# Performance work log

Hardware: AMD Instinct MI355X
Metric: run time of the kernel (lower is better)

Reference implementation:

```python
import jax, jax.numpy as jnp
import numpy as np

B, T, D = 64, 32, 256
NFC = 2 * D          # num_inputs_fc = 512
DIMS = [4 * D, NFC, NFC // 2, NFC // 4, NFC // 8, 4]  # last layer padded to 4 outs
H = 4                # camera, rot, trans, plane heads stacked


def setup_inputs() -> dict:
    key = jax.random.key(0)
    ks = jax.random.split(key, 12)
    inp = {
        "emb": jax.random.normal(ks[0], (B, T, D), dtype=jnp.float32),
        # each of n0, n1 in [1,16] so n0+n1 <= T=32 and no divide-by-zero
        "num_planes": jax.random.randint(ks[1], (B, 2), 1, 17, dtype=jnp.int32),
    }
    for i in range(5):
        fan_in = DIMS[i]
        scale = 1.0 / np.sqrt(fan_in)
        inp[f"w{i}"] = jax.random.uniform(ks[2 + 2 * i], (H, DIMS[i], DIMS[i + 1]),
                                           minval=-scale, maxval=scale, dtype=jnp.float32)
        inp[f"b{i}"] = jax.random.uniform(ks[3 + 2 * i], (H, DIMS[i + 1]),
                                           minval=-scale, maxval=scale, dtype=jnp.float32)
    return inp


def _forward(emb, num_planes, w0, b0, w1, b1, w2, b2, w3, b3, w4, b4):
    Bs, Ts, Ds = emb.shape
    n0 = num_planes[:, 0]
    n1 = num_planes[:, 1]
    idx = jnp.arange(Ts)
    # img1 global feature: mean of tokens t < n0 (original zeroes t>=n0 then sums / n0)
    m1 = (idx[None, :] < n0[:, None])                                  # (B,T) bool
    g1 = (emb * m1[..., None].astype(emb.dtype)).sum(1) / n0[:, None].astype(emb.dtype)
    # img2 global feature: mean of tokens n0 <= t < n0+n1
    in2 = (idx[None, :] >= n0[:, None]) & (idx[None, :] < (n0 + n1)[:, None])  # (B,T)
    g2 = (emb * in2[..., None].astype(emb.dtype)).sum(1) / n1[:, None].astype(emb.dtype)
    # pairwise concat: [emb_i, emb_j, g1, g2] -> (B,T,T,4D)
    ei = jnp.broadcast_to(emb[:, :, None, :], (Bs, Ts, Ts, Ds))
    ej = jnp.broadcast_to(emb[:, None, :, :], (Bs, Ts, Ts, Ds))
    g1b = jnp.broadcast_to(g1[:, None, None, :], (Bs, Ts, Ts, Ds))
    g2b = jnp.broadcast_to(g2[:, None, None, :], (Bs, Ts, Ts, Ds))
    cat = jnp.concatenate([ei, ej, g1b, g2b], axis=-1)
    # 4 stacked MLP heads (camera, rot, trans, plane); final layer padded to 4 outputs
    h = jax.nn.relu(jnp.einsum('btsd,hdk->hbtsk', cat, w0) + b0[:, None, None, None, :])
    h = jax.nn.relu(jnp.einsum('hbtsd,hdk->hbtsk', h, w1) + b1[:, None, None, None, :])
    h = jax.nn.relu(jnp.einsum('hbtsd,hdk->hbtsk', h, w2) + b2[:, None, None, None, :])
    h = jax.nn.relu(jnp.einsum('hbtsd,hdk->hbtsk', h, w3) + b3[:, None, None, None, :])
    h = jnp.einsum('hbtsd,hdk->hbtsk', h, w4) + b4[:, None, None, None, :]  # (4,B,T,T,4)
    camera = h[0, ..., 0]            # (B,T,T)
    rot = h[1]                       # (B,T,T,4)
    trans = h[2, ..., :3]            # (B,T,T,3)
    plane_corr = jax.nn.sigmoid(h[3, ..., 0])  # (B,T,T)
    # valid pairs: row i < n0, col j in [n0, n0+n1)  (== ~padding_mask)
    valid = m1[:, :, None] & in2[:, None, :]                           # (B,T,T) bool
    v = valid.astype(emb.dtype)
    pf = (n0 * n1).astype(emb.dtype)
    camera_corr = jax.nn.sigmoid((camera * v).sum((1, 2)) / pf)        # (B,)
    rot_res = (rot * v[..., None]).sum((1, 2)) / pf[:, None]           # (B,4)
    trans_res = (trans * v[..., None]).sum((1, 2)) / pf[:, None]       # (B,3)
    return camera_corr, rot_res, trans_res, plane_corr, valid


def reference(emb, num_planes, w0, b0, w1, b1, w2, b2, w3, b3, w4, b4):
    return _forward(emb, num_planes, w0, b0, w1, b1, w2, b2, w3, b3, w4, b4)
```

## Files before the change

kernel.cpp:

```cpp
#include <hip/hip_runtime.h>

typedef float f32x4 __attribute__((ext_vector_type(4)));
typedef short short8 __attribute__((ext_vector_type(8)));
typedef unsigned short ushort_t;
typedef unsigned int uint_t;

constexpr int O_CAM   = 0;
constexpr int O_ROT   = 64;
constexpr int O_TRANS = 320;
constexpr int O_PLANE = 512;
constexpr int O_VALID = 66048;

constexpr size_t B_G1   = 0;
constexpr size_t B_G2   = 65536;
constexpr size_t B_ACC  = 131072;
constexpr size_t B_ABF  = 133120;
constexpr size_t B_CBF  = 8521728;
constexpr size_t B_BT1  = 16910336;
constexpr size_t B_BT2  = 17958912;
constexpr size_t B_BT3  = 18221056;
constexpr size_t B_BT0F = 18286592;

__device__ __forceinline__ ushort_t f2bf(float f) {
    uint_t u = __float_as_uint(f);
    return (ushort_t)((u + 0x7FFFu + ((u >> 16) & 1u)) >> 16);
}

__device__ __forceinline__ uint_t cvt_pk_bf16(float lo, float hi) {
    uint_t r;
    asm("v_cvt_pk_bf16_f32 %0, %1, %2" : "=v"(r) : "v"(lo), "v"(hi));
    return r;
}

__device__ __forceinline__ uint_t bfadd2_relu(uint_t a, uint_t c) {
    const float lo = __uint_as_float(a << 16) + __uint_as_float(c << 16);
    const float hi = __uint_as_float(a & 0xffff0000u) + __uint_as_float(c & 0xffff0000u);
    return cvt_pk_bf16(fmaxf(lo, 0.f), fmaxf(hi, 0.f));
}

__global__ __launch_bounds__(256) void k_prepA(
    const float* __restrict__ emb, const int* __restrict__ np_,
    const float* __restrict__ w0, ushort_t* __restrict__ bt0f,
    float* __restrict__ g1, float* __restrict__ g2)
{
    const int l = threadIdx.x & 63;
    const int c = blockIdx.x * 4 + (threadIdx.x >> 6);
    if (c >= 4160) return;
    if (c < 4096) {
        const int h = c >> 10, ks = (c >> 5) & 31, nt = c & 31;
        const int n = nt*16 + (l & 15);
        const int d0 = ks*32 + ((l >> 4) << 3);
        short8 o;
        #pragma unroll
        for (int j = 0; j < 8; ++j)
            o[j] = (short)f2bf(w0[((size_t)h*1024 + d0 + j)*512 + n]);
        *(short8*)(bt0f + (size_t)c*512 + (size_t)l*8) = o;
    } else {
        const int b = c - 4096;
        const int n0 = np_[2*b], n1 = np_[2*b+1];
        const float* e = emb + (size_t)b*8192;
        #pragma unroll
        for (int dd = 0; dd < 4; ++dd) {
            const int d = l + 64*dd;
            float a1 = 0.f, a2 = 0.f;
            for (int t = 0; t < 32; ++t) {
                float v = e[t*256 + d];
                if (t < n0) a1 += v;
                else if (t < n0 + n1) a2 += v;
            }
            g1[b*256 + d] = a1 / n0;
            g2[b*256 + d] = a2 / n1;
        }
    }
}

__global__ __launch_bounds__(256) void k_ACp(
    const float* __restrict__ emb, const ushort_t* __restrict__ bt0f,
    const float* __restrict__ g1, const float* __restrict__ g2,
    const float* __restrict__ b0,
    ushort_t* __restrict__ Abf, ushort_t* __restrict__ Cbf,
    const float* __restrict__ w1, const float* __restrict__ w2, const float* __restrict__ w3,
    ushort_t* __restrict__ bt1, ushort_t* __restrict__ bt2, ushort_t* __restrict__ bt3,
    const int* __restrict__ np_, float* __restrict__ accz, float* __restrict__ out)
{
    const int tid = threadIdx.x;
    const int l = tid & 63;

    if (blockIdx.x >= 512) {
        int c = (blockIdx.x - 512) * 4 + (tid >> 6);
        if (c >= 1409) return;
        if (c < 1344) {
            const float* w; ushort_t* dst; int K, N;
            if (c < 1024)      {           w = w1; dst = bt1 + (size_t)c*512; K = 512; N = 256; }
            else if (c < 1280) { c -= 1024; w = w2; dst = bt2 + (size_t)c*512; K = 256; N = 128; }
            else               { c -= 1280; w = w3; dst = bt3 + (size_t)c*512; K = 128; N = 64;  }
            const int NT = N/16, KS_NT = (K/32)*NT;
            const int h = c / KS_NT, rem = c % KS_NT, ks = rem / NT, nt = rem % NT;
            const int n = nt*16 + (l & 15);
            const int d0 = ks*32 + ((l >> 4) << 3);
            short8 o;
            #pragma unroll
            for (int j = 0; j < 8; ++j)
                o[j] = (short)f2bf(w[((size_t)(h*K + d0 + j))*N + n]);
            *(short8*)(dst + (size_t)l*8) = o;
        } else if (c == 1344) {
            #pragma unroll
            for (int i = 0; i < 8; ++i) accz[l*8 + i] = 0.f;
        } else {
            const int b = c - 1345;
            const int n0 = np_[2*b], n1 = np_[2*b+1];
            float* dst = out + O_VALID + b*1024;
            #pragma unroll
            for (int i = 0; i < 16; ++i) {
                const int j = l*16 + i;
                const int t = j >> 5, s = j & 31;
                dst[j] = (t < n0 && s >= n0 && s < n0 + n1) ? 1.f : 0.f;
            }
        }
        return;
    }

    const int b = blockIdx.x & 63, hc = blockIdx.x >> 6;
    const int h = hc >> 1, isC = hc & 1;
    const int w4w = tid >> 6;
    const int lrow = l & 15, lko = l >> 4;

    __shared__ __align__(16) char es[16384];
    __shared__ __align__(16) ushort_t gs[512];

    {
        const float* eb = emb + (size_t)b*8192;
        #pragma unroll
        for (int j = 0; j < 16; ++j) {
            const int flat = j*256 + tid;
            const int row = flat >> 7, cp = flat & 127;
            const float2 v = *(const float2*)(eb + row*256 + cp*2);
            const uint_t p = (uint_t)f2bf(v.x) | ((uint_t)f2bf(v.y) << 16);
            const int byte = (row*512 + cp*4) ^ ((row & 7) << 4);
            *(uint_t*)(es + byte) = p;
        }
    }
    if (!isC && tid < 64) {
        const float* src = (tid < 32) ? (g1 + b*256 + tid*8) : (g2 + b*256 + (tid - 32)*8);
        const float4 v0 = *(const float4*)(src);
        const float4 v1 = *(const float4*)(src + 4);
        short8 o;
        o[0] = (short)f2bf(v0.x); o[1] = (short)f2bf(v0.y);
        o[2] = (short)f2bf(v0.z); o[3] = (short)f2bf(v0.w);
        o[4] = (short)f2bf(v1.x); o[5] = (short)f2bf(v1.y);
        o[6] = (short)f2bf(v1.z); o[7] = (short)f2bf(v1.w);
        *(short8*)(gs + tid*8) = o;
    }
    __syncthreads();

    f32x4 acc[2][8];
    #pragma unroll
    for (int mt = 0; mt < 2; ++mt)
        #pragma unroll
        for (int nt = 0; nt < 8; ++nt) acc[mt][nt] = (f32x4){0.f,0.f,0.f,0.f};

    const ushort_t* basef = bt0f + (size_t)h*(32*32*512) + (size_t)(w4w*8)*512 + (size_t)l*8;

    {
        const int ksE0 = isC ? 8 : 0;
        for (int kk = 0; kk < 8; ++kk) {
            short8 bfv[8];
            const ushort_t* bp = basef + (size_t)(ksE0 + kk)*16384;
            #pragma unroll
            for (int nt = 0; nt < 8; ++nt) bfv[nt] = *(const short8*)(bp + nt*512);
            const int o = (lrow*512 + kk*64 + lko*16) ^ ((lrow & 7) << 4);
            const short8 a0 = *(const short8*)(es + o);
            const short8 a1 = *(const short8*)(es + o + 8192);
            __builtin_amdgcn_s_setprio(1);
            #pragma unroll
            for (int nt = 0; nt < 8; ++nt) {
                acc[0][nt] = __builtin_amdgcn_mfma_f32_16x16x32_bf16(a0, bfv[nt], acc[0][nt], 0, 0, 0);
                acc[1][nt] = __builtin_amdgcn_mfma_f32_16x16x32_bf16(a1, bfv[nt], acc[1][nt], 0, 0, 0);
            }
            __builtin_amdgcn_s_setprio(0);
        }
    }
    if (!isC) {
        for (int kk = 0; kk < 16; ++kk) {
            short8 bfv[8];
            const ushort_t* bp = basef + (size_t)(16 + kk)*16384;
            #pragma unroll
            for (int nt = 0; nt < 8; ++nt) bfv[nt] = *(const short8*)(bp + nt*512);
            const short8 ag = *(const short8*)(gs + kk*32 + lko*8);
            __builtin_amdgcn_s_setprio(1);
            #pragma unroll
            for (int nt = 0; nt < 8; ++nt) {
                acc[0][nt] = __builtin_amdgcn_mfma_f32_16x16x32_bf16(ag, bfv[nt], acc[0][nt], 0, 0, 0);
                acc[1][nt] = __builtin_amdgcn_mfma_f32_16x16x32_bf16(ag, bfv[nt], acc[1][nt], 0, 0, 0);
            }
            __builtin_amdgcn_s_setprio(0);
        }
    }

    ushort_t* dst = (isC ? Cbf : Abf) + (size_t)(h*64 + b)*32*512;
    #pragma unroll
    for (int nt = 0; nt < 8; ++nt) {
        const int col = (w4w*8 + nt)*16 + lrow;
        const float g = isC ? 0.f : b0[h*512 + col];
        #pragma unroll
        for (int mt = 0; mt < 2; ++mt)
            #pragma unroll
            for (int r = 0; r < 4; ++r) {
                const int row = mt*16 + lko*4 + r;
                dst[row*512 + col] = f2bf(acc[mt][nt][r] + g);
            }
    }
}

__global__ __launch_bounds__(512, 8) void k_mlp(
    const ushort_t* __restrict__ Abf, const ushort_t* __restrict__ Cbf,
    const ushort_t* __restrict__ bt1, const ushort_t* __restrict__ bt2, const ushort_t* __restrict__ bt3,
    const float* __restrict__ b1, const float* __restrict__ b2, const float* __restrict__ b3,
    const float* __restrict__ w4, const float* __restrict__ b4,
    const int* __restrict__ np_, float* __restrict__ out, float* __restrict__ accbuf)
{
    const int x = blockIdx.x;
    const bool isH3 = (x < 1024);
    int h, b, t0;
    int n0 = 0, n1 = 0;
    if (isH3) {
        h = 3; b = x >> 4; t0 = (x & 15) * 2;
    } else {
        const int y = x - 1024;
        h = y >> 8; b = (y >> 2) & 63; t0 = (y & 3) * 4;
        n0 = np_[2*b]; n1 = np_[2*b+1];
        if (t0 >= n0) return;
    }

    __shared__ __align__(16) char smem[49152];
    char* X   = smem;
    char* X2  = smem + 32768;
    char* X3b = smem;
    float* X4 = (float*)(smem + 8192);

    const int tid = threadIdx.x;
    const int l = tid & 63, w = tid >> 6;
    const int lrow = l & 15, lko = l >> 4;
    const size_t hb = (size_t)(h*64 + b);
    const uint4* Arows = (const uint4*)(Abf + hb*32*512);
    const uint4* Crows = (const uint4*)(Cbf + hb*32*512);

    f32x4 acc1[4][2];
    #pragma unroll
    for (int mt = 0; mt < 4; ++mt)
        #pragma unroll
        for (int nt = 0; nt < 2; ++nt) acc1[mt][nt] = (f32x4){0.f,0.f,0.f,0.f};

    const ushort_t* bp1 = bt1 + (size_t)(h*256 + w*2)*512 + (size_t)l*8;

    for (int p = 0; p < 2; ++p) {
        if (p) __syncthreads();
        #pragma unroll
        for (int i = 0; i < 4; ++i) {
            const int flat = i*512 + tid;
            const int row = flat >> 5, q4 = flat & 31;
            int trow, crow;
            if (isH3) { trow = t0 + (row >> 5); crow = row & 31; }
            else      { trow = t0 + (row >> 4); crow = n0 + (row & 15); }
            const uint4 aa = Arows[(size_t)trow*64 + p*32 + q4];
            const uint4 cc = Crows[(size_t)crow*64 + p*32 + q4];
            uint4 v;
            v.x = bfadd2_relu(aa.x, cc.x);
            v.y = bfadd2_relu(aa.y, cc.y);
            v.z = bfadd2_relu(aa.z, cc.z);
            v.w = bfadd2_relu(aa.w, cc.w);
            *(uint4*)(X + ((row*512 + q4*16) ^ ((row & 7) << 4))) = v;
        }
        __syncthreads();

        const ushort_t* bpp = bp1 + (size_t)p*8*8192;
        for (int ks = 0; ks < 8; ++ks) {
            const short8 bf0 = *(const short8*)(bpp + (size_t)ks*8192);
            const short8 bf1 = *(const short8*)(bpp + (size_t)ks*8192 + 512);
            __builtin_amdgcn_s_setprio(1);
            #pragma unroll
            for (int mt = 0; mt < 4; ++mt) {
                const short8 a0 = *(const short8*)(X + (((mt*16 + lrow)*512 + ks*64 + lko*16) ^ ((lrow & 7) << 4)));
                acc1[mt][0] = __builtin_amdgcn_mfma_f32_16x16x32_bf16(a0, bf0, acc1[mt][0], 0, 0, 0);
                acc1[mt][1] = __builtin_amdgcn_mfma_f32_16x16x32_bf16(a0, bf1, acc1[mt][1], 0, 0, 0);
            }
            __builtin_amdgcn_s_setprio(0);
        }
    }
    __syncthreads();

    #pragma unroll
    for (int nt = 0; nt < 2; ++nt) {
        const int col = (w*2 + nt)*16 + lrow;
        const float bias = b1[h*256 + col];
        #pragma unroll
        for (int mt = 0; mt < 4; ++mt)
            #pragma unroll
            for (int r = 0; r < 4; ++r) {
                const int row = mt*16 + lko*4 + r;
                const float v = fmaxf(acc1[mt][nt][r] + bias, 0.f);
                *(ushort_t*)(X + ((row*512 + col*2) ^ ((row & 7) << 4))) =
                    (ushort_t)cvt_pk_bf16(v, v);
            }
    }
    __syncthreads();

    f32x4 acc2[4];
    #pragma unroll
    for (int mt = 0; mt < 4; ++mt) acc2[mt] = (f32x4){0.f,0.f,0.f,0.f};
    {
        const ushort_t* bp = bt2 + (size_t)(h*64 + w)*512 + (size_t)l*8;
        for (int ks = 0; ks < 8; ++ks) {
            const short8 bf = *(const short8*)(bp + (size_t)ks*4096);
            __builtin_amdgcn_s_setprio(1);
            #pragma unroll
            for (int mt = 0; mt < 4; ++mt) {
                const short8 a0 = *(const short8*)(X + (((mt*16 + lrow)*512 + ks*64 + lko*16) ^ ((lrow & 7) << 4)));
                acc2[mt] = __builtin_amdgcn_mfma_f32_16x16x32_bf16(a0, bf, acc2[mt], 0, 0, 0);
            }
            __builtin_amdgcn_s_setprio(0);
        }
    }
    {
        const int col = w*16 + lrow;
        const float bias = b2[h*128 + col];
        #pragma unroll
        for (int mt = 0; mt < 4; ++mt)
            #pragma unroll
            for (int r = 0; r < 4; ++r) {
                const int row = mt*16 + lko*4 + r;
                const float v = fmaxf(acc2[mt][r] + bias, 0.f);
                *(ushort_t*)(X2 + ((row*256 + col*2) ^ ((row & 7) << 4))) =
                    (ushort_t)cvt_pk_bf16(v, v);
            }
    }
    __syncthreads();

    const int mhalf = w >> 2;
    f32x4 acc3[2];
    acc3[0] = (f32x4){0.f,0.f,0.f,0.f};
    acc3[1] = (f32x4){0.f,0.f,0.f,0.f};
    {
        const ushort_t* bp = bt3 + (size_t)(h*16 + (w & 3))*512 + (size_t)l*8;
        for (int ks = 0; ks < 4; ++ks) {
            const short8 bf = *(const short8*)(bp + (size_t)ks*2048);
            __builtin_amdgcn_s_setprio(1);
            #pragma unroll
            for (int mi = 0; mi < 2; ++mi) {
                const int mt = mhalf*2 + mi;
                const short8 a0 = *(const short8*)(X2 + (((mt*16 + lrow)*256 + ks*64 + lko*16) ^ ((lrow & 7) << 4)));
                acc3[mi] = __builtin_amdgcn_mfma_f32_16x16x32_bf16(a0, bf, acc3[mi], 0, 0, 0);
            }
            __builtin_amdgcn_s_setprio(0);
        }
    }
    {
        const int col = (w & 3)*16 + lrow;
        const float bias = b3[h*64 + col];
        #pragma unroll
        for (int mi = 0; mi < 2; ++mi) {
            const int mt = mhalf*2 + mi;
            #pragma unroll
            for (int r = 0; r < 4; ++r) {
                const int row = mt*16 + lko*4 + r;
                const float v = fmaxf(acc3[mi][r] + bias, 0.f);
                *(ushort_t*)(X3b + ((row*128 + col*2) ^ ((row & 7) << 4))) =
                    (ushort_t)cvt_pk_bf16(v, v);
            }
        }
    }
    __syncthreads();

    if (tid < 256) {
        const int row = tid >> 2, o = tid & 3;
        const float* w4g = w4 + (size_t)h*256 + o;
        float a = b4[h*4 + o];
        #pragma unroll
        for (int dd = 0; dd < 16; ++dd) {
            const int dbase = ((row + dd) & 15) * 4;
            const uint2 u = *(const uint2*)(X3b + ((row*128 + dbase*2) ^ ((row & 7) << 4)));
            const float f0 = __uint_as_float(u.x << 16);
            const float f1 = __uint_as_float(u.x & 0xffff0000u);
            const float f2 = __uint_as_float(u.y << 16);
            const float f3 = __uint_as_float(u.y & 0xffff0000u);
            a = fmaf(f0, w4g[(dbase + 0)*4], a);
            a = fmaf(f1, w4g[(dbase + 1)*4], a);
            a = fmaf(f2, w4g[(dbase + 2)*4], a);
            a = fmaf(f3, w4g[(dbase + 3)*4], a);
        }
        X4[row*4 + o] = a;
    }
    __syncthreads();

    if (isH3) {
        if (tid < 64) {
            const int tq = tid >> 5, s = tid & 31;
            out[O_PLANE + b*1024 + (t0 + tq)*32 + s] = 1.f / (1.f + expf(-X4[tid*4]));
        }
    } else {
        const int nj = (h == 0) ? 1 : ((h == 1) ? 4 : 3);
        const int j = w;
        if (j < nj) {
            const int tq = l >> 4, sr = l & 15;
            const bool valid = ((t0 + tq) < n0) && (sr < n1);
            float v = valid ? X4[l*4 + j] : 0.f;
            #pragma unroll
            for (int off = 32; off > 0; off >>= 1) v += __shfl_down(v, off);
            if (l == 0) {
                const int slot = (h == 0) ? 0 : ((h == 1) ? 1 + j : 5 + j);
                atomicAdd(&accbuf[b*8 + slot], v);
            }
        }
    }
}

__global__ __launch_bounds__(512) void k_final(
    const int* __restrict__ np_, const float* __restrict__ acc, float* __restrict__ out)
{
    const int tid = threadIdx.x;
    const int b = tid >> 3, sl = tid & 7;
    const int n0 = np_[2*b], n1 = np_[2*b+1];
    const float pf = (float)(n0 * n1);
    const float v = acc[b*8 + sl] / pf;
    if (sl == 0)      out[O_CAM + b] = 1.f / (1.f + expf(-v));
    else if (sl <= 4) out[O_ROT + b*4 + (sl - 1)] = v;
    else              out[O_TRANS + b*3 + (sl - 5)] = v;
}

extern "C" void kernel_launch(void* const* d_in, const int* in_sizes, int n_in,
                              void* d_out, int out_size, void* d_ws, size_t ws_size,
                              hipStream_t stream) {
    (void)in_sizes; (void)n_in; (void)out_size; (void)ws_size;
    const float* emb = (const float*)d_in[0];
    const int*   np_ = (const int*)d_in[1];
    const float* w0  = (const float*)d_in[2];
    const float* b0  = (const float*)d_in[3];
    const float* w1  = (const float*)d_in[4];
    const float* b1  = (const float*)d_in[5];
    const float* w2  = (const float*)d_in[6];
    const float* b2  = (const float*)d_in[7];
    const float* w3  = (const float*)d_in[8];
    const float* b3  = (const float*)d_in[9];
    const float* w4  = (const float*)d_in[10];
    const float* b4  = (const float*)d_in[11];

    char* W = (char*)d_ws;
    float* out = (float*)d_out;
    float*    g1   = (float*)(W + B_G1);
    float*    g2   = (float*)(W + B_G2);
    float*    acc  = (float*)(W + B_ACC);
    ushort_t* Abf  = (ushort_t*)(W + B_ABF);
    ushort_t* Cbf  = (ushort_t*)(W + B_CBF);
    ushort_t* bt1  = (ushort_t*)(W + B_BT1);
    ushort_t* bt2  = (ushort_t*)(W + B_BT2);
    ushort_t* bt3  = (ushort_t*)(W + B_BT3);
    ushort_t* bt0f = (ushort_t*)(W + B_BT0F);

    k_prepA<<<1040, 256, 0, stream>>>(emb, np_, w0, bt0f, g1, g2);
    k_ACp<<<865, 256, 0, stream>>>(emb, bt0f, g1, g2, b0, Abf, Cbf,
                                   w1, w2, w3, bt1, bt2, bt3, np_, acc, out);
    k_mlp<<<1792, 512, 0, stream>>>(Abf, Cbf, bt1, bt2, bt3,
                                    b1, b2, b3, w4, b4, np_, out, acc);
    k_final<<<1, 512, 0, stream>>>(np_, acc, out);
}
```

Baseline: 98.25 us.

## Use MFMA for final layer, stage full layer-1 input, double-buffer weight loads

The final 64->4 layer moves from scalar FMAs over global fp32 weights to a bf16 MFMA, using a new pre-packed, zero-padded bt4 weight buffer built in k_ACp. The layer-1 A tile is now staged into shared memory in one pass over all of K (64KB LDS), which removes the two-phase loop and its extra barrier. B-fragment loads for layers 1 and 2 are double-buffered in registers. In exchange, LDS use grows from 48KB to 64KB and the launch-bound occupancy hint drops from 8 to 2, which may reduce the number of resident waves and the latency hiding they provide.

After: 85.25 us. -13.2%, faster.

```diff
diff --git a/kernel.cpp b/kernel.cpp
--- a/kernel.cpp
+++ b/kernel.cpp
@@ -20,6 +20,7 @@
 constexpr size_t B_BT2  = 17958912;
 constexpr size_t B_BT3  = 18221056;
 constexpr size_t B_BT0F = 18286592;
+constexpr size_t B_BT4  = 22480896;
 
 __device__ __forceinline__ ushort_t f2bf(float f) {
     uint_t u = __float_as_uint(f);
@@ -80,7 +81,9 @@
     const float* __restrict__ b0,
     ushort_t* __restrict__ Abf, ushort_t* __restrict__ Cbf,
     const float* __restrict__ w1, const float* __restrict__ w2, const float* __restrict__ w3,
+    const float* __restrict__ w4,
     ushort_t* __restrict__ bt1, ushort_t* __restrict__ bt2, ushort_t* __restrict__ bt3,
+    ushort_t* __restrict__ bt4,
     const int* __restrict__ np_, float* __restrict__ accz, float* __restrict__ out)
 {
     const int tid = threadIdx.x;
@@ -88,7 +91,7 @@
 
     if (blockIdx.x >= 512) {
         int c = (blockIdx.x - 512) * 4 + (tid >> 6);
-        if (c >= 1409) return;
+        if (c >= 1417) return;
         if (c < 1344) {
             const float* w; ushort_t* dst; int K, N;
             if (c < 1024)      {           w = w1; dst = bt1 + (size_t)c*512; K = 512; N = 256; }
@@ -106,7 +109,7 @@
         } else if (c == 1344) {
             #pragma unroll
             for (int i = 0; i < 8; ++i) accz[l*8 + i] = 0.f;
-        } else {
+        } else if (c < 1409) {
             const int b = c - 1345;
             const int n0 = np_[2*b], n1 = np_[2*b+1];
             float* dst = out + O_VALID + b*1024;
@@ -116,6 +119,16 @@
                 const int t = j >> 5, s = j & 31;
                 dst[j] = (t < n0 && s >= n0 && s < n0 + n1) ? 1.f : 0.f;
             }
+        } else {
+            const int u = c - 1409;
+            const int h = u >> 1, ks = u & 1;
+            const int n = l & 15;
+            const int d0 = ks*32 + ((l >> 4) << 3);
+            short8 o;
+            #pragma unroll
+            for (int j = 0; j < 8; ++j)
+                o[j] = (n < 4) ? (short)f2bf(w4[(size_t)h*256 + (d0 + j)*4 + n]) : (short)0;
+            *(short8*)(bt4 + ((size_t)u*64 + l)*8) = o;
         }
         return;
     }
@@ -212,11 +225,12 @@
     }
 }
 
-__global__ __launch_bounds__(512, 8) void k_mlp(
+__global__ __launch_bounds__(512, 2) void k_mlp(
     const ushort_t* __restrict__ Abf, const ushort_t* __restrict__ Cbf,
-    const ushort_t* __restrict__ bt1, const ushort_t* __restrict__ bt2, const ushort_t* __restrict__ bt3,
+    const ushort_t* __restrict__ bt1, const ushort_t* __restrict__ bt2,
+    const ushort_t* __restrict__ bt3, const ushort_t* __restrict__ bt4,
     const float* __restrict__ b1, const float* __restrict__ b2, const float* __restrict__ b3,
-    const float* __restrict__ w4, const float* __restrict__ b4,
+    const float* __restrict__ b4,
     const int* __restrict__ np_, float* __restrict__ out, float* __restrict__ accbuf)
 {
     const int x = blockIdx.x;
@@ -232,11 +246,10 @@
         if (t0 >= n0) return;
     }
 
-    __shared__ __align__(16) char smem[49152];
+    __shared__ __align__(16) char smem[65536];
     char* X   = smem;
-    char* X2  = smem + 32768;
-    char* X3b = smem;
-    float* X4 = (float*)(smem + 8192);
+    char* X2  = smem + 49152;
+    char* X3b = smem + 32768;
 
     const int tid = threadIdx.x;
     const int l = tid & 63, w = tid >> 6;
@@ -245,47 +258,51 @@
     const uint4* Arows = (const uint4*)(Abf + hb*32*512);
     const uint4* Crows = (const uint4*)(Cbf + hb*32*512);
 
+    const ushort_t* bp1 = bt1 + (size_t)(h*256 + w*2)*512 + (size_t)l*8;
+    short8 bb[2][2];
+    bb[0][0] = *(const short8*)(bp1);
+    bb[0][1] = *(const short8*)(bp1 + 512);
+
+    #pragma unroll
+    for (int i = 0; i < 8; ++i) {
+        const int flat = i*512 + tid;
+        const int row = flat >> 6, q4 = flat & 63;
+        int trow, crow;
+        if (isH3) { trow = t0 + (row >> 5); crow = row & 31; }
+        else      { trow = t0 + (row >> 4); crow = n0 + (row & 15); }
+        const uint4 aa = Arows[(size_t)trow*64 + q4];
+        const uint4 cc = Crows[(size_t)crow*64 + q4];
+        uint4 v;
+        v.x = bfadd2_relu(aa.x, cc.x);
+        v.y = bfadd2_relu(aa.y, cc.y);
+        v.z = bfadd2_relu(aa.z, cc.z);
+        v.w = bfadd2_relu(aa.w, cc.w);
+        *(uint4*)(X + ((row*1024 + q4*16) ^ ((row & 7) << 4))) = v;
+    }
+    __syncthreads();
+
     f32x4 acc1[4][2];
     #pragma unroll
     for (int mt = 0; mt < 4; ++mt)
         #pragma unroll
         for (int nt = 0; nt < 2; ++nt) acc1[mt][nt] = (f32x4){0.f,0.f,0.f,0.f};
 
-    const ushort_t* bp1 = bt1 + (size_t)(h*256 + w*2)*512 + (size_t)l*8;
-
-    for (int p = 0; p < 2; ++p) {
-        if (p) __syncthreads();
-        #pragma unroll
-        for (int i = 0; i < 4; ++i) {
-            const int flat = i*512 + tid;
-            const int row = flat >> 5, q4 = flat & 31;
-            int trow, crow;
-            if (isH3) { trow = t0 + (row >> 5); crow = row & 31; }
-            else      { trow = t0 + (row >> 4); crow = n0 + (row & 15); }
-            const uint4 aa = Arows[(size_t)trow*64 + p*32 + q4];
-            const uint4 cc = Crows[(size_t)crow*64 + p*32 + q4];
-            uint4 v;
-            v.x = bfadd2_relu(aa.x, cc.x);
-            v.y = bfadd2_relu(aa.y, cc.y);
-            v.z = bfadd2_relu(aa.z, cc.z);
-            v.w = bfadd2_relu(aa.w, cc.w);
-            *(uint4*)(X + ((row*512 + q4*16) ^ ((row & 7) << 4))) = v;
-        }
-        __syncthreads();
-
-        const ushort_t* bpp = bp1 + (size_t)p*8*8192;
-        for (int ks = 0; ks < 8; ++ks) {
-            const short8 bf0 = *(const short8*)(bpp + (size_t)ks*8192);
-            const short8 bf1 = *(const short8*)(bpp + (size_t)ks*8192 + 512);
-            __builtin_amdgcn_s_setprio(1);
-            #pragma unroll
-            for (int mt = 0; mt < 4; ++mt) {
-                const short8 a0 = *(const short8*)(X + (((mt*16 + lrow)*512 + ks*64 + lko*16) ^ ((lrow & 7) << 4)));
-                acc1[mt][0] = __builtin_amdgcn_mfma_f32_16x16x32_bf16(a0, bf0, acc1[mt][0], 0, 0, 0);
-                acc1[mt][1] = __builtin_amdgcn_mfma_f32_16x16x32_bf16(a0, bf1, acc1[mt][1], 0, 0, 0);
-            }
-            __builtin_amdgcn_s_setprio(0);
-        }
+    #pragma unroll
+    for (int ks = 0; ks < 16; ++ks) {
+        if (ks < 15) {
+            bb[(ks+1)&1][0] = *(const short8*)(bp1 + (size_t)(ks+1)*8192);
+            bb[(ks+1)&1][1] = *(const short8*)(bp1 + (size_t)(ks+1)*8192 + 512);
+        }
+        const short8 bf0 = bb[ks&1][0];
+        const short8 bf1 = bb[ks&1][1];
+        __builtin_amdgcn_s_setprio(1);
+        #pragma unroll
+        for (int mt = 0; mt < 4; ++mt) {
+            const short8 a0 = *(const short8*)(X + (((mt*16 + lrow)*1024 + ks*64 + lko*16) ^ ((lrow & 7) << 4)));
+            acc1[mt][0] = __builtin_amdgcn_mfma_f32_16x16x32_bf16(a0, bf0, acc1[mt][0], 0, 0, 0);
+            acc1[mt][1] = __builtin_amdgcn_mfma_f32_16x16x32_bf16(a0, bf1, acc1[mt][1], 0, 0, 0);
+        }
+        __builtin_amdgcn_s_setprio(0);
     }
     __syncthreads();
 
@@ -310,13 +327,16 @@
     for (int mt = 0; mt < 4; ++mt) acc2[mt] = (f32x4){0.f,0.f,0.f,0.f};
     {
         const ushort_t* bp = bt2 + (size_t)(h*64 + w)*512 + (size_t)l*8;
+        short8 b2b[2];
+        b2b[0] = *(const short8*)(bp);
+        #pragma unroll
         for (int ks = 0; ks < 8; ++ks) {
-            const short8 bf = *(const short8*)(bp + (size_t)ks*4096);
+            if (ks < 7) b2b[(ks+1)&1] = *(const short8*)(bp + (size_t)(ks+1)*4096);
             __builtin_amdgcn_s_setprio(1);
             #pragma unroll
             for (int mt = 0; mt < 4; ++mt) {
                 const short8 a0 = *(const short8*)(X + (((mt*16 + lrow)*512 + ks*64 + lko*16) ^ ((lrow & 7) << 4)));
-                acc2[mt] = __builtin_amdgcn_mfma_f32_16x16x32_bf16(a0, bf, acc2[mt], 0, 0, 0);
+                acc2[mt] = __builtin_amdgcn_mfma_f32_16x16x32_bf16(a0, b2b[ks&1], acc2[mt], 0, 0, 0);
             }
             __builtin_amdgcn_s_setprio(0);
         }
@@ -342,6 +362,7 @@
     acc3[1] = (f32x4){0.f,0.f,0.f,0.f};
     {
         const ushort_t* bp = bt3 + (size_t)(h*16 + (w & 3))*512 + (size_t)l*8;
+        #pragma unroll
         for (int ks = 0; ks < 4; ++ks) {
             const short8 bf = *(const short8*)(bp + (size_t)ks*2048);
             __builtin_amdgcn_s_setprio(1);
@@ -371,43 +392,42 @@
     }
     __syncthreads();
 
-    if (tid < 256) {
-        const int row = tid >> 2, o = tid & 3;
-        const float* w4g = w4 + (size_t)h*256 + o;
-        float a = b4[h*4 + o];
-        #pragma unroll
-        for (int dd = 0; dd < 16; ++dd) {
-            const int dbase = ((row + dd) & 15) * 4;
-            const uint2 u = *(const uint2*)(X3b + ((row*128 + dbase*2) ^ ((row & 7) << 4)));
-            const float f0 = __uint_as_float(u.x << 16);
-            const float f1 = __uint_as_float(u.x & 0xffff0000u);
-            const float f2 = __uint_as_float(u.y << 16);
-            const float f3 = __uint_as_float(u.y & 0xffff0000u);
-            a = fmaf(f0, w4g[(dbase + 0)*4], a);
-            a = fmaf(f1, w4g[(dbase + 1)*4], a);
-            a = fmaf(f2, w4g[(dbase + 2)*4], a);
-            a = fmaf(f3, w4g[(dbase + 3)*4], a);
-        }
-        X4[row*4 + o] = a;
-    }
-    __syncthreads();
-
-    if (isH3) {
-        if (tid < 64) {
-            const int tq = tid >> 5, s = tid & 31;
-            out[O_PLANE + b*1024 + (t0 + tq)*32 + s] = 1.f / (1.f + expf(-X4[tid*4]));
-        }
-    } else {
-        const int nj = (h == 0) ? 1 : ((h == 1) ? 4 : 3);
-        const int j = w;
-        if (j < nj) {
-            const int tq = l >> 4, sr = l & 15;
-            const bool valid = ((t0 + tq) < n0) && (sr < n1);
-            float v = valid ? X4[l*4 + j] : 0.f;
-            #pragma unroll
-            for (int off = 32; off > 0; off >>= 1) v += __shfl_down(v, off);
-            if (l == 0) {
-                const int slot = (h == 0) ? 0 : ((h == 1) ? 1 + j : 5 + j);
+    if (w < 4) {
+        const int mt = w;
+        f32x4 acc4 = (f32x4){0.f,0.f,0.f,0.f};
+        const ushort_t* bp = bt4 + (size_t)(h*2)*512 + (size_t)l*8;
+        #pragma unroll
+        for (int ks = 0; ks < 2; ++ks) {
+            const short8 bf = *(const short8*)(bp + (size_t)ks*512);
+            const short8 a0 = *(const short8*)(X3b + (((mt*16 + lrow)*128 + ks*64 + lko*16) ^ ((lrow & 7) << 4)));
+            acc4 = __builtin_amdgcn_mfma_f32_16x16x32_bf16(a0, bf, acc4, 0, 0, 0);
+        }
+        const float bias = b4[h*4 + (lrow & 3)];
+        #pragma unroll
+        for (int r = 0; r < 4; ++r) acc4[r] += bias;
+
+        if (isH3) {
+            if (lrow == 0) {
+                #pragma unroll
+                for (int r = 0; r < 4; ++r) {
+                    const int row = mt*16 + lko*4 + r;
+                    out[O_PLANE + b*1024 + (t0 + (row >> 5))*32 + (row & 31)] =
+                        1.f / (1.f + expf(-acc4[r]));
+                }
+            }
+        } else {
+            const int nj = (h == 0) ? 1 : ((h == 1) ? 4 : 3);
+            float v = 0.f;
+            #pragma unroll
+            for (int r = 0; r < 4; ++r) {
+                const int row = mt*16 + lko*4 + r;
+                const int tq = row >> 4, sr = row & 15;
+                if ((t0 + tq) < n0 && sr < n1) v += acc4[r];
+            }
+            v += __shfl_down(v, 32);
+            v += __shfl_down(v, 16);
+            if (lko == 0 && lrow < nj) {
+                const int slot = (h == 0) ? 0 : ((h == 1) ? 1 + lrow : 5 + lrow);
                 atomicAdd(&accbuf[b*8 + slot], v);
             }
         }
@@ -455,11 +475,12 @@
     ushort_t* bt2  = (ushort_t*)(W + B_BT2);
     ushort_t* bt3  = (ushort_t*)(W + B_BT3);
     ushort_t* bt0f = (ushort_t*)(W + B_BT0F);
+    ushort_t* bt4  = (ushort_t*)(W + B_BT4);
 
     k_prepA<<<1040, 256, 0, stream>>>(emb, np_, w0, bt0f, g1, g2);
-    k_ACp<<<865, 256, 0, stream>>>(emb, bt0f, g1, g2, b0, Abf, Cbf,
-                                   w1, w2, w3, bt1, bt2, bt3, np_, acc, out);
-    k_mlp<<<1792, 512, 0, stream>>>(Abf, Cbf, bt1, bt2, bt3,
-                                    b1, b2, b3, w4, b4, np_, out, acc);
+    k_ACp<<<867, 256, 0, stream>>>(emb, bt0f, g1, g2, b0, Abf, Cbf,
+                                   w1, w2, w3, w4, bt1, bt2, bt3, bt4, np_, acc, out);
+    k_mlp<<<1792, 512, 0, stream>>>(Abf, Cbf, bt1, bt2, bt3, bt4,
+                                    b1, b2, b3, b4, np_, out, acc);
     k_final<<<1, 512, 0, stream>>>(np_, acc, out);
 }
```
